# Performance work log

Hardware: AMD Instinct MI355X
Metric: run time of the kernel (lower is better)

Reference implementation:

```python
import jax, jax.numpy as jnp
import numpy as np

B, N, D, H, E, C = 32, 1024, 256, 256, 256, 256
K = 128          # top-k retained clusters = C // top_ratio
TEMP = 0.1
EPS = 1e-15


def _l2norm(x, eps=1e-12):
    n = jnp.linalg.norm(x, axis=-1, keepdims=True)
    return x / jnp.maximum(n, eps)


def _dense_sage(x, adj, Wr, br, Wo):
    # PyG DenseSAGEConv: mean-aggregate neighbors, lin_rel + lin_root, l2-normalize
    deg = jnp.clip(jnp.sum(adj, axis=-1, keepdims=True), 1.0, None)
    agg = jnp.matmul(adj, x) / deg                      # [B,N,D]
    out = agg @ Wr + br + x @ Wo                         # [B,N,H]
    return _l2norm(out)


def _sage_block(x, adj, Wr, br, Wo, Wl, bl):
    h = jax.nn.relu(_dense_sage(x, adj, Wr, br, Wo))
    return h @ Wl + bl


def setup_inputs() -> dict:
    key = jax.random.key(0)
    ks = jax.random.split(key, 12)
    sc = 0.05
    return {
        "x": jax.random.normal(ks[0], (B, N, D), jnp.float32),
        "adj": jax.random.uniform(ks[1], (B, N, N), jnp.float32),
        # pool branch (out = C clusters)
        "Wr_p": jax.random.normal(ks[2], (D, H), jnp.float32) * sc,
        "br_p": jnp.zeros((H,), jnp.float32),
        "Wo_p": jax.random.normal(ks[3], (D, H), jnp.float32) * sc,
        "Wl_p": jax.random.normal(ks[4], (H, C), jnp.float32) * sc,
        "bl_p": jnp.zeros((C,), jnp.float32),
        # embed branch (out = E features)
        "Wr_e": jax.random.normal(ks[5], (D, H), jnp.float32) * sc,
        "br_e": jnp.zeros((H,), jnp.float32),
        "Wo_e": jax.random.normal(ks[6], (D, H), jnp.float32) * sc,
        "Wl_e": jax.random.normal(ks[7], (H, E), jnp.float32) * sc,
        "bl_e": jnp.zeros((E,), jnp.float32),
    }


def reference(x, adj, Wr_p, br_p, Wo_p, Wl_p, bl_p, Wr_e, br_e, Wo_e, Wl_e, bl_e):
    s_logits = _sage_block(x, adj, Wr_p, br_p, Wo_p, Wl_p, bl_p)   # [B,N,C]
    node_x = _sage_block(x, adj, Wr_e, br_e, Wo_e, Wl_e, bl_e)     # [B,N,E]

    s = jax.nn.softmax(s_logits, axis=-1)

    # soft top-k cluster retain: sigmoid gate around the k-th largest column mass
    scores = jnp.sum(s, axis=1)                                    # [B,C]
    thresh = jax.lax.top_k(scores, K)[0][:, -1]                    # [B]
    gate = jax.nn.sigmoid((scores - thresh[:, None]) / TEMP)       # [B,C]
    s = s * gate[:, None, :]

    # pooled features / adjacency
    xp = jnp.einsum('bnc,bnd->bcd', s, node_x)                     # [B,C,E]
    sTa = jnp.einsum('bnc,bnm->bcm', s, adj)                       # [B,C,N]
    adj_p = jnp.einsum('bcm,bmk->bck', sTa, s)                     # [B,C,C]

    # link prediction loss: ||A - S S^T||_F / numel(A)
    ssT = jnp.einsum('bnc,bmc->bnm', s, s)
    link = jnp.linalg.norm(adj - ssT) / adj.size

    # entropy loss over assignments
    ent = jnp.mean(jnp.sum(-s * jnp.log(s + EPS), axis=-1))

    # cluster (orthogonality) loss: ||S^T S / ||S^T S||_F - I/sqrt(C)||_F
    sts = jnp.einsum('bnc,bnk->bck', s, s)                         # [B,C,C]
    sts_n = sts / jnp.maximum(
        jnp.linalg.norm(sts, axis=(-2, -1), keepdims=True), 1e-12)
    eye = jnp.eye(C, dtype=s.dtype) / jnp.sqrt(jnp.asarray(C, s.dtype))
    clu = jnp.mean(jnp.linalg.norm(sts_n - eye, axis=(-2, -1)))

    # adjacency reconstruction loss: ||A - S A_pool S^T||_F / numel(A)
    recon_adj = jnp.einsum('bnc,bck,bmk->bnm', s, adj_p, s)
    recon = jnp.linalg.norm(adj - recon_adj) / adj.size

    return (xp, adj_p, s, link, ent, clu, recon, node_x)
```

## Files before the change

### kernel.cpp

```cpp
#include <hip/hip_runtime.h>
#include <hip/hip_bf16.h>
#include <math.h>


typedef short bf16x8 __attribute__((ext_vector_type(8)));
typedef float f32x4 __attribute__((ext_vector_type(4)));

__device__ inline void gl_lds16(const void* g, void* l) {
    __builtin_amdgcn_global_load_lds(
        (const __attribute__((address_space(1))) void*)g,
        (__attribute__((address_space(3))) void*)l, 16, 0, 0);
}

__device__ inline unsigned short f2b(float f) {
    union { __hip_bfloat16 h; unsigned short u; } cv;
    cv.h = __float2bfloat16(f);
    return cv.u;
}
__device__ inline float b2f(unsigned short u) {
    union { unsigned short u; __hip_bfloat16 h; } cv;
    cv.u = u;
    return __bfloat162float(cv.h);
}

__global__ __launch_bounds__(256) void adjconv_kernel(
    const float* __restrict__ adj, unsigned short* __restrict__ adj_bf,
    float* __restrict__ deginv, float* __restrict__ asq_part) {
    __shared__ float sq_red[4];
    const int tid = threadIdx.x;
    const int wave = tid >> 6, lane = tid & 63;
    const long long row = (long long)blockIdx.x * 4 + wave;
    const float* ip = adj + row * 1024;
    unsigned short* op = adj_bf + row * 1024;
    float sum = 0.f, sq = 0.f;
#pragma unroll
    for (int i = 0; i < 4; ++i) {
        const float4 v = *(const float4*)(ip + i * 256 + lane * 4);
        ushort4 h;
        h.x = f2b(v.x); h.y = f2b(v.y); h.z = f2b(v.z); h.w = f2b(v.w);
        *(ushort4*)(op + i * 256 + lane * 4) = h;
        sum += v.x + v.y + v.z + v.w;
        sq = fmaf(v.x, v.x, sq);
        sq = fmaf(v.y, v.y, sq);
        sq = fmaf(v.z, v.z, sq);
        sq = fmaf(v.w, v.w, sq);
    }
#pragma unroll
    for (int off = 32; off > 0; off >>= 1) {
        sum += __shfl_xor(sum, off);
        sq  += __shfl_xor(sq, off);
    }
    if (lane == 0) {
        deginv[row] = 1.0f / fmaxf(sum, 1.0f);
        sq_red[wave] = sq;
    }
    __syncthreads();
    if (tid == 0)
        asq_part[blockIdx.x] = sq_red[0] + sq_red[1] + sq_red[2] + sq_red[3];
}

__global__ __launch_bounds__(256) void convt_kernel(
    const float* __restrict__ in, long long sIn, int ldin,
    unsigned short* __restrict__ outN, long long sN,
    unsigned short* __restrict__ outT, long long sT, int ldT,
    float* __restrict__ sqpart) {
    __shared__ float tile[64][65];
    __shared__ float sred[256];
    const int tid = threadIdx.x;
    const long long bz = blockIdx.z;
    const int rowBase = blockIdx.y * 64, colBase = blockIdx.x * 64;
    const float* ip = in + bz * sIn;
    float sq = 0.f;
#pragma unroll
    for (int i = 0; i < 4; ++i) {
        int r = (tid >> 4) * 4 + i;
        const float4 v = *(const float4*)(ip + (long long)(rowBase + r) * ldin + colBase + (tid & 15) * 4);
        tile[r][(tid & 15) * 4 + 0] = v.x;
        tile[r][(tid & 15) * 4 + 1] = v.y;
        tile[r][(tid & 15) * 4 + 2] = v.z;
        tile[r][(tid & 15) * 4 + 3] = v.w;
        if (outN) {
            ushort4 h;
            h.x = f2b(v.x); h.y = f2b(v.y); h.z = f2b(v.z); h.w = f2b(v.w);
            *(ushort4*)(outN + bz * sN + (long long)(rowBase + r) * ldin + colBase + (tid & 15) * 4) = h;
        }
        if (sqpart) sq += v.x * v.x + v.y * v.y + v.z * v.z + v.w * v.w;
    }
    __syncthreads();
    if (outT) {
#pragma unroll
        for (int i = 0; i < 4; ++i) {
            int oc = (tid >> 4) * 4 + i;
            ushort4 h;
            h.x = f2b(tile[(tid & 15) * 4 + 0][oc]);
            h.y = f2b(tile[(tid & 15) * 4 + 1][oc]);
            h.z = f2b(tile[(tid & 15) * 4 + 2][oc]);
            h.w = f2b(tile[(tid & 15) * 4 + 3][oc]);
            *(ushort4*)(outT + bz * sT + (long long)(colBase + oc) * ldT + rowBase + (tid & 15) * 4) = h;
        }
    }
    if (sqpart) {
        sred[tid] = sq;
        __syncthreads();
        for (int k = 128; k > 0; k >>= 1) {
            if (tid < k) sred[tid] += sred[tid + k];
            __syncthreads();
        }
        if (tid == 0)
            sqpart[((long long)bz * gridDim.y + blockIdx.y) * gridDim.x + blockIdx.x] = sred[0];
    }
}

__global__ __launch_bounds__(256) void tbf16_kernel(
    const unsigned short* __restrict__ in, long long sIn, int ldin,
    unsigned short* __restrict__ outT, long long sT, int ldT) {
    __shared__ unsigned short tile[64][68];
    const int tid = threadIdx.x;
    const long long bz = blockIdx.z;
    const int rowBase = blockIdx.y * 64, colBase = blockIdx.x * 64;
    const unsigned short* ip = in + bz * sIn;
#pragma unroll
    for (int i = 0; i < 4; ++i) {
        int r = (tid >> 4) * 4 + i, c4 = (tid & 15) * 4;
        ushort4 v = *(const ushort4*)(ip + (long long)(rowBase + r) * ldin + colBase + c4);
        tile[r][c4 + 0] = v.x; tile[r][c4 + 1] = v.y;
        tile[r][c4 + 2] = v.z; tile[r][c4 + 3] = v.w;
    }
    __syncthreads();
#pragma unroll
    for (int i = 0; i < 4; ++i) {
        int oc = (tid >> 4) * 4 + i;
        ushort4 h;
        h.x = tile[(tid & 15) * 4 + 0][oc];
        h.y = tile[(tid & 15) * 4 + 1][oc];
        h.z = tile[(tid & 15) * 4 + 2][oc];
        h.w = tile[(tid & 15) * 4 + 3][oc];
        *(ushort4*)(outT + bz * sT + (long long)(colBase + oc) * ldT + rowBase + (tid & 15) * 4) = h;
    }
}

struct WPtrs { const float* in[6]; unsigned short* out[6]; };
__global__ __launch_bounds__(256) void wconv_kernel(WPtrs wp) {
    __shared__ float tile[64][65];
    const int tid = threadIdx.x;
    const float* in = wp.in[blockIdx.z];
    unsigned short* out = wp.out[blockIdx.z];
    const int rowBase = blockIdx.y * 64, colBase = blockIdx.x * 64;
#pragma unroll
    for (int i = 0; i < 4; ++i) {
        int r = (tid >> 4) * 4 + i;
        const float4 v = *(const float4*)(in + (long long)(rowBase + r) * 256 + colBase + (tid & 15) * 4);
        tile[r][(tid & 15) * 4 + 0] = v.x;
        tile[r][(tid & 15) * 4 + 1] = v.y;
        tile[r][(tid & 15) * 4 + 2] = v.z;
        tile[r][(tid & 15) * 4 + 3] = v.w;
    }
    __syncthreads();
#pragma unroll
    for (int i = 0; i < 4; ++i) {
        int oc = (tid >> 4) * 4 + i;
        ushort4 h;
        h.x = f2b(tile[(tid & 15) * 4 + 0][oc]);
        h.y = f2b(tile[(tid & 15) * 4 + 1][oc]);
        h.z = f2b(tile[(tid & 15) * 4 + 2][oc]);
        h.w = f2b(tile[(tid & 15) * 4 + 3][oc]);
        *(ushort4*)(out + (long long)(colBase + oc) * 256 + rowBase + (tid & 15) * 4) = h;
    }
}

struct GemmP {
    const unsigned short* A1; long long sA1; int lda1; int K1;
    const unsigned short* B1; long long sB1; int ldb1;
    const unsigned short* A2; long long sA2; int lda2; int K2;
    const unsigned short* B2; long long sB2; int ldb2;
    float* outF; long long sF;
    unsigned short* outH; long long sH;
    int ldc;
    const float* bias;
    const float* rowscale; long long sRS;
    const float* dotT; long long sDot;
    float* dot_part;
};

__global__ __launch_bounds__(256) void gemm_mfma(GemmP p) {
    __shared__ short As[2][128 * 32];
    __shared__ short Bs[2][128 * 32];
    __shared__ float dred[256];
    const int tid = threadIdx.x;
    const int wave = tid >> 6, lane = tid & 63;
    const int quad = lane >> 4, l15 = lane & 15;
    const int wm = (wave & 1) * 64, wn = (wave >> 1) * 64;
    const long long bz = blockIdx.z;
    const int rowBase = blockIdx.y * 128, colBase = blockIdx.x * 128;
    const int srow = tid >> 2;
    const int skg = (((tid & 3) ^ ((srow >> 1) & 3)) * 8);
    const int rsw = (l15 >> 1) & 3;

    const int n1 = p.K1 >> 5;
    const int n2 = p.A2 ? (p.K2 >> 5) : 0;
    const int nTot = n1 + n2;

    const unsigned short* A1p = p.A1 + bz * p.sA1;
    const unsigned short* B1p = p.B1 + bz * p.sB1;
    const unsigned short* A2p = p.A2 ? p.A2 + bz * p.sA2 : nullptr;
    const unsigned short* B2p = p.B2 ? p.B2 + bz * p.sB2 : nullptr;

    auto stage = [&](int t, int buf) {
        const unsigned short *Ao, *Bo; int lda, ldb, ko;
        if (t < n1) { Ao = A1p; Bo = B1p; lda = p.lda1; ldb = p.ldb1; ko = t * 32; }
        else        { Ao = A2p; Bo = B2p; lda = p.lda2; ldb = p.ldb2; ko = (t - n1) * 32; }
        char* la = (char*)As + buf * 8192 + wave * 1024;
        char* lb = (char*)Bs + buf * 8192 + wave * 1024;
        gl_lds16(Ao + (long long)(rowBase + srow) * lda + ko + skg, la);
        gl_lds16(Ao + (long long)(rowBase + 64 + srow) * lda + ko + skg, la + 4096);
        gl_lds16(Bo + (long long)(colBase + srow) * ldb + ko + skg, lb);
        gl_lds16(Bo + (long long)(colBase + 64 + srow) * ldb + ko + skg, lb + 4096);
    };

    f32x4 acc[4][4] = {{{0.f}}};
    stage(0, 0);
    __syncthreads();
    int cur = 0;
    for (int t = 0; t < nTot; ++t) {
        if (t + 1 < nTot) stage(t + 1, cur ^ 1);
        const short* Ab = As[cur];
        const short* Bb = Bs[cur];
        bf16x8 af[4], bf[4];
#pragma unroll
        for (int i = 0; i < 4; ++i)
            af[i] = *(const bf16x8*)(Ab + (wm + i * 16 + l15) * 32 + (quad ^ rsw) * 8);
#pragma unroll
        for (int j = 0; j < 4; ++j)
            bf[j] = *(const bf16x8*)(Bb + (wn + j * 16 + l15) * 32 + (quad ^ rsw) * 8);
#pragma unroll
        for (int i = 0; i < 4; ++i)
#pragma unroll
            for (int j = 0; j < 4; ++j)
                acc[i][j] = __builtin_amdgcn_mfma_f32_16x16x32_bf16(af[i], bf[j], acc[i][j], 0, 0, 0);
        __syncthreads();
        cur ^= 1;
    }

    float* oF = p.outF ? p.outF + bz * p.sF : nullptr;
    unsigned short* oH = p.outH ? p.outH + bz * p.sH : nullptr;
    const float* dT = p.dotT ? p.dotT + bz * p.sDot : nullptr;
    float bcol[4];
#pragma unroll
    for (int j = 0; j < 4; ++j)
        bcol[j] = p.bias ? p.bias[colBase + wn + j * 16 + l15] : 0.0f;
    const float* rs = p.rowscale ? p.rowscale + bz * p.sRS : nullptr;
    float dacc = 0.f;
#pragma unroll
    for (int i = 0; i < 4; ++i) {
#pragma unroll
        for (int r = 0; r < 4; ++r) {
            int row = rowBase + wm + i * 16 + quad * 4 + r;
            float sc = rs ? rs[row] : 1.0f;
            long long ro = (long long)row * p.ldc;
#pragma unroll
            for (int j = 0; j < 4; ++j) {
                int col = colBase + wn + j * 16 + l15;
                float v = (acc[i][j][r] + bcol[j]) * sc;
                if (oF) oF[ro + col] = v;
                if (oH) oH[ro + col] = f2b(v);
                if (dT) dacc = fmaf(v, dT[(long long)col * p.ldc + row], dacc);
            }
        }
    }
    if (p.dot_part) {
        dred[tid] = dacc;
        __syncthreads();
        for (int k = 128; k > 0; k >>= 1) {
            if (tid < k) dred[tid] += dred[tid + k];
            __syncthreads();
        }
        if (tid == 0)
            p.dot_part[((long long)bz * gridDim.y + blockIdx.y) * gridDim.x + blockIdx.x] = dred[0];
    }
}

__global__ __launch_bounds__(256) void sts_clu_mfma(
    const unsigned short* __restrict__ sT, unsigned short* __restrict__ gout,
    float* __restrict__ ssq_part, float* __restrict__ tr_part) {
    __shared__ short As[2][128 * 32];
    __shared__ short Bs[2][128 * 32];
    __shared__ float red[2][256];
    const int tid = threadIdx.x;
    const int wave = tid >> 6, lane = tid & 63;
    const int quad = lane >> 4, l15 = lane & 15;
    const int wm = (wave & 1) * 64, wn = (wave >> 1) * 64;
    const long long bz = blockIdx.z;
    const unsigned short* S = sT + bz * 262144;
    const int rowBase = blockIdx.y * 128, colBase = blockIdx.x * 128;
    const int srow = tid >> 2;
    const int skg = (((tid & 3) ^ ((srow >> 1) & 3)) * 8);
    const int rsw = (l15 >> 1) & 3;

    auto stage = [&](int t, int buf) {
        int ko = t * 32;
        char* la = (char*)As + buf * 8192 + wave * 1024;
        char* lb = (char*)Bs + buf * 8192 + wave * 1024;
        gl_lds16(S + (long long)(rowBase + srow) * 1024 + ko + skg, la);
        gl_lds16(S + (long long)(rowBase + 64 + srow) * 1024 + ko + skg, la + 4096);
        gl_lds16(S + (long long)(colBase + srow) * 1024 + ko + skg, lb);
        gl_lds16(S + (long long)(colBase + 64 + srow) * 1024 + ko + skg, lb + 4096);
    };

    f32x4 acc[4][4] = {{{0.f}}};
    stage(0, 0);
    __syncthreads();
    int cur = 0;
    for (int t = 0; t < 32; ++t) {
        if (t + 1 < 32) stage(t + 1, cur ^ 1);
        const short* Ab = As[cur];
        const short* Bb = Bs[cur];
        bf16x8 af[4], bf[4];
#pragma unroll
        for (int i = 0; i < 4; ++i)
            af[i] = *(const bf16x8*)(Ab + (wm + i * 16 + l15) * 32 + (quad ^ rsw) * 8);
#pragma unroll
        for (int j = 0; j < 4; ++j)
            bf[j] = *(const bf16x8*)(Bb + (wn + j * 16 + l15) * 32 + (quad ^ rsw) * 8);
#pragma unroll
        for (int i = 0; i < 4; ++i)
#pragma unroll
            for (int j = 0; j < 4; ++j)
                acc[i][j] = __builtin_amdgcn_mfma_f32_16x16x32_bf16(af[i], bf[j], acc[i][j], 0, 0, 0);
        __syncthreads();
        cur ^= 1;
    }
    unsigned short* go = gout + bz * 65536;
    float ssq = 0.f, tr = 0.f;
#pragma unroll
    for (int i = 0; i < 4; ++i)
#pragma unroll
        for (int r = 0; r < 4; ++r) {
            int row = rowBase + wm + i * 16 + quad * 4 + r;
#pragma unroll
            for (int j = 0; j < 4; ++j) {
                int col = colBase + wn + j * 16 + l15;
                float v = acc[i][j][r];
                go[(long long)row * 256 + col] = f2b(v);
                ssq = fmaf(v, v, ssq);
                if (row == col) tr += v;
            }
        }
    red[0][tid] = ssq;
    red[1][tid] = tr;
    __syncthreads();
    for (int k = 128; k > 0; k >>= 1) {
        if (tid < k) {
            red[0][tid] += red[0][tid + k];
            red[1][tid] += red[1][tid + k];
        }
        __syncthreads();
    }
    if (tid == 0) {
        int bid = (int)(blockIdx.z * 4 + blockIdx.y * 2 + blockIdx.x);
        ssq_part[bid] = red[0][0];
        tr_part[bid] = red[1][0];
    }
}

__global__ __launch_bounds__(256) void dot_bf_kernel(const unsigned short* __restrict__ a,
                                                     const unsigned short* __restrict__ b,
                                                     float* __restrict__ part) {
    __shared__ float red[256];
    int tid = threadIdx.x;
    long long base = (long long)blockIdx.x * 8192;
    float acc = 0.f;
#pragma unroll
    for (int i = 0; i < 8; ++i) {
        long long off = base + i * 1024 + tid * 4;
        ushort4 va = *(const ushort4*)(a + off);
        ushort4 vb = *(const ushort4*)(b + off);
        acc = fmaf(b2f(va.x), b2f(vb.x), acc);
        acc = fmaf(b2f(va.y), b2f(vb.y), acc);
        acc = fmaf(b2f(va.z), b2f(vb.z), acc);
        acc = fmaf(b2f(va.w), b2f(vb.w), acc);
    }
    red[tid] = acc;
    __syncthreads();
    for (int k = 128; k > 0; k >>= 1) {
        if (tid < k) red[tid] += red[tid + k];
        __syncthreads();
    }
    if (tid == 0) part[blockIdx.x] = red[0];
}

__global__ __launch_bounds__(256) void l2relu_bf_kernel(unsigned short* __restrict__ buf) {
    __shared__ float red[256];
    long long row = blockIdx.x;
    int tid = threadIdx.x;
    float v = b2f(buf[row * 256 + tid]);
    red[tid] = v * v;
    __syncthreads();
    for (int k = 128; k > 0; k >>= 1) {
        if (tid < k) red[tid] += red[tid + k];
        __syncthreads();
    }
    float rn = 1.0f / fmaxf(sqrtf(red[0]), 1e-12f);
    buf[row * 256 + tid] = f2b(fmaxf(v * rn, 0.0f));
}

__global__ __launch_bounds__(256) void smstat_kernel(
    const float* __restrict__ s, float* __restrict__ rowmax,
    float* __restrict__ rowrden, float* __restrict__ scores) {
    __shared__ float sacc[4][256];
    const int tid = threadIdx.x;
    const int wave = tid >> 6, lane = tid & 63;
    const int b = blockIdx.x >> 5;
    const long long row0 = (long long)blockIdx.x * 32;
    float c0 = 0.f, c1 = 0.f, c2 = 0.f, c3 = 0.f;
#pragma unroll
    for (int q = 0; q < 8; ++q) {
        long long row = row0 + wave * 8 + q;
        const float4 v = *(const float4*)(s + row * 256 + lane * 4);
        float m = fmaxf(fmaxf(v.x, v.y), fmaxf(v.z, v.w));
#pragma unroll
        for (int off = 32; off > 0; off >>= 1) m = fmaxf(m, __shfl_xor(m, off));
        float e0 = expf(v.x - m), e1 = expf(v.y - m);
        float e2 = expf(v.z - m), e3 = expf(v.w - m);
        float den = e0 + e1 + e2 + e3;
#pragma unroll
        for (int off = 32; off > 0; off >>= 1) den += __shfl_xor(den, off);
        float rd = 1.0f / den;
        if (lane == 0) { rowmax[row] = m; rowrden[row] = rd; }
        c0 = fmaf(e0, rd, c0); c1 = fmaf(e1, rd, c1);
        c2 = fmaf(e2, rd, c2); c3 = fmaf(e3, rd, c3);
    }
    sacc[wave][lane * 4 + 0] = c0;
    sacc[wave][lane * 4 + 1] = c1;
    sacc[wave][lane * 4 + 2] = c2;
    sacc[wave][lane * 4 + 3] = c3;
    __syncthreads();
    float t0 = sacc[0][tid] + sacc[1][tid] + sacc[2][tid] + sacc[3][tid];
    atomicAdd(&scores[b * 256 + tid], t0);
}

__global__ __launch_bounds__(256) void topk_kernel(const float* __restrict__ scores,
                                                   float* __restrict__ thresh) {
    __shared__ float vals[256];
    int b = blockIdx.x, tid = threadIdx.x;
    float v = scores[b * 256 + tid];
    vals[tid] = v;
    __syncthreads();
    int rank = 0;
    for (int j = 0; j < 256; ++j) {
        float u = vals[j];
        rank += (u > v) || (u == v && j < tid);
    }
    if (rank == 127) thresh[b] = v;
}

__global__ __launch_bounds__(256) void gate_kernel(const float* __restrict__ scores,
                                                   const float* __restrict__ thresh,
                                                   float* __restrict__ gate) {
    int b = blockIdx.x, c = threadIdx.x;
    float z = (scores[b * 256 + c] - thresh[b]) * 10.0f;
    gate[b * 256 + c] = 1.0f / (1.0f + expf(-z));
}

__global__ __launch_bounds__(256) void gatefin_kernel(
    float* __restrict__ s, const float* __restrict__ rowmax,
    const float* __restrict__ rowrden, const float* __restrict__ gate,
    unsigned short* __restrict__ sbf, unsigned short* __restrict__ sT,
    float* __restrict__ ent_part) {
    __shared__ float tile[64][65];
    __shared__ float red[256];
    const int tid = threadIdx.x;
    const long long bz = blockIdx.z;
    const int rowBase = blockIdx.y * 64, colBase = blockIdx.x * 64;
    const int c4 = (tid & 15) * 4;
    const float g0 = gate[bz * 256 + colBase + c4 + 0];
    const float g1 = gate[bz * 256 + colBase + c4 + 1];
    const float g2 = gate[bz * 256 + colBase + c4 + 2];
    const float g3 = gate[bz * 256 + colBase + c4 + 3];
    float ent = 0.f;
#pragma unroll
    for (int i = 0; i < 4; ++i) {
        int r = (tid >> 4) * 4 + i;
        long long grow = bz * 1024 + rowBase + r;
        float4 v = *(const float4*)(s + grow * 256 + colBase + c4);
        float m = rowmax[grow], rd = rowrden[grow];
        float p0 = expf(v.x - m) * rd * g0;
        float p1 = expf(v.y - m) * rd * g1;
        float p2 = expf(v.z - m) * rd * g2;
        float p3 = expf(v.w - m) * rd * g3;
        float4 pv; pv.x = p0; pv.y = p1; pv.z = p2; pv.w = p3;
        *(float4*)(s + grow * 256 + colBase + c4) = pv;
        ushort4 h;
        h.x = f2b(p0); h.y = f2b(p1); h.z = f2b(p2); h.w = f2b(p3);
        *(ushort4*)(sbf + grow * 256 + colBase + c4) = h;
        tile[r][c4 + 0] = p0; tile[r][c4 + 1] = p1;
        tile[r][c4 + 2] = p2; tile[r][c4 + 3] = p3;
        ent -= p0 * logf(p0 + 1e-15f) + p1 * logf(p1 + 1e-15f) +
               p2 * logf(p2 + 1e-15f) + p3 * logf(p3 + 1e-15f);
    }
    __syncthreads();
#pragma unroll
    for (int i = 0; i < 4; ++i) {
        int oc = (tid >> 4) * 4 + i;
        ushort4 h;
        h.x = f2b(tile[c4 + 0][oc]);
        h.y = f2b(tile[c4 + 1][oc]);
        h.z = f2b(tile[c4 + 2][oc]);
        h.w = f2b(tile[c4 + 3][oc]);
        *(ushort4*)(sT + bz * 262144 + (long long)(colBase + oc) * 1024 + rowBase + c4) = h;
    }
    red[tid] = ent;
    __syncthreads();
    for (int k = 128; k > 0; k >>= 1) {
        if (tid < k) red[tid] += red[tid + k];
        __syncthreads();
    }
    if (tid == 0)
        ent_part[((long long)bz * gridDim.y + blockIdx.y) * gridDim.x + blockIdx.x] = red[0];
}

__global__ __launch_bounds__(256) void finalize_kernel(const float* __restrict__ ent_part,
                                                       const float* __restrict__ asq_part,
                                                       const float* __restrict__ psq_part,
                                                       const float* __restrict__ sdot_part,
                                                       const float* __restrict__ trq_part,
                                                       const float* __restrict__ ssq_part,
                                                       const float* __restrict__ tr_part,
                                                       float* __restrict__ scal) {
    __shared__ float red[7][256];
    int tid = threadIdx.x;
    float e = 0.f, asq = 0.f, psq = 0.f, sd = 0.f, tq = 0.f, clu = 0.f, ssqa = 0.f;
    for (int i = tid; i < 2048; i += 256) e += ent_part[i];
    for (int i = tid; i < 8192; i += 256) asq += asq_part[i];
    for (int i = tid; i < 512; i += 256) psq += psq_part[i];
    for (int i = tid; i < 1024; i += 256) sd += sdot_part[i];
    if (tid < 128) tq = trq_part[tid];
    if (tid < 32) {
        float ssq = 0.f, tr = 0.f;
#pragma unroll
        for (int i = 0; i < 4; ++i) {
            ssq += ssq_part[tid * 4 + i];
            tr  += tr_part[tid * 4 + i];
        }
        ssqa = ssq;
        float fro = fmaxf(sqrtf(ssq), 1e-12f);
        float val = ssq / (fro * fro) - tr / (8.0f * fro) + 1.0f;
        clu = sqrtf(fmaxf(val, 0.0f));
    }
    red[0][tid] = e; red[1][tid] = asq; red[2][tid] = psq; red[3][tid] = sd;
    red[4][tid] = tq; red[5][tid] = clu; red[6][tid] = ssqa;
    __syncthreads();
    for (int k = 128; k > 0; k >>= 1) {
        if (tid < k) {
#pragma unroll
            for (int q = 0; q < 7; ++q) red[q][tid] += red[q][tid + k];
        }
        __syncthreads();
    }
    if (tid == 0) {
        const float numel = 33554432.0f;
        float linksq  = red[1][0] - 2.0f * red[3][0] + red[6][0];
        float reconsq = red[1][0] - 2.0f * red[2][0] + red[4][0];
        scal[0] = sqrtf(fmaxf(linksq, 0.0f)) / numel;
        scal[1] = red[0][0] / 32768.0f;
        scal[2] = red[5][0] / 32.0f;
        scal[3] = sqrtf(fmaxf(reconsq, 0.0f)) / numel;
    }
}

extern "C" void kernel_launch(void* const* d_in, const int* in_sizes, int n_in,
                              void* d_out, int out_size, void* d_ws, size_t ws_size,
                              hipStream_t stream) {
    const float* x    = (const float*)d_in[0];
    const float* adj  = (const float*)d_in[1];
    const float* Wr_p = (const float*)d_in[2];
    const float* br_p = (const float*)d_in[3];
    const float* Wo_p = (const float*)d_in[4];
    const float* Wl_p = (const float*)d_in[5];
    const float* bl_p = (const float*)d_in[6];
    const float* Wr_e = (const float*)d_in[7];
    const float* br_e = (const float*)d_in[8];
    const float* Wo_e = (const float*)d_in[9];
    const float* Wl_e = (const float*)d_in[10];
    const float* bl_e = (const float*)d_in[11];

    float* out    = (float*)d_out;
    float* xp     = out;
    float* adj_p  = out + 2097152;
    float* s      = out + 4194304;
    float* scal   = out + 12582912;
    float* node_x = out + 12582916;

    char* w = (char*)d_ws;
    float* degsum     = (float*)w; w += 32768 * 4;
    float* scores     = (float*)w; w += 8192 * 4;
    float* thresh     = (float*)w; w += 256 * 4;
    float* gatep      = (float*)w; w += 8192 * 4;
    float* ent_part   = (float*)w; w += 32768 * 4;
    float* asq_part   = (float*)w; w += 8192 * 4;
    float* psq_part   = (float*)w; w += 512 * 4;
    float* sdot_part  = (float*)w; w += 1024 * 4;
    float* trq_part   = (float*)w; w += 256 * 4;
    float* ssq_part   = (float*)w; w += 256 * 4;
    float* tr_part    = (float*)w; w += 256 * 4;
    unsigned short* WT   = (unsigned short*)w; w += 6LL * 65536 * 2;
    unsigned short* bufA = (unsigned short*)w; w += 33554432LL * 2;
    unsigned short* bufB = (unsigned short*)w; w += 8388608LL * 2;
    unsigned short* bufC = (unsigned short*)w; w += 8388608LL * 2;
    unsigned short* bufD = (unsigned short*)w; w += 8388608LL * 2;
    unsigned short* bufE = (unsigned short*)w; w += 8388608LL * 2;
    unsigned short* bufF = (unsigned short*)w; w += 8388608LL * 2;
    unsigned short* bufG = (unsigned short*)w; w += 8388608LL * 2;
    unsigned short* bufH = (unsigned short*)w; w += 2097152LL * 2;

    unsigned short* G_bf  = bufB;
    unsigned short* PT_bf = bufB + 2097152;
    float*          M1    = (float*)(bufB + 4194304);
    float* rowmax  = degsum;
    float* rowrden = (float*)bufH;

    hipMemsetAsync(scores, 0, 8192 * sizeof(float), stream);

    adjconv_kernel<<<8192, 256, 0, stream>>>(adj, bufA, degsum, asq_part);

    convt_kernel<<<dim3(4, 16, 32), 256, 0, stream>>>(
        x, 262144LL, 256, bufB, 262144LL, bufC, 262144LL, 1024, nullptr);

    WPtrs wp;
    wp.in[0] = Wr_p; wp.in[1] = Wo_p; wp.in[2] = Wl_p;
    wp.in[3] = Wr_e; wp.in[4] = Wo_e; wp.in[5] = Wl_e;
    for (int i = 0; i < 6; ++i) wp.out[i] = WT + (long long)i * 65536;
    wconv_kernel<<<dim3(4, 4, 6), 256, 0, stream>>>(wp);

    GemmP g;
    g = {};
    g.A1 = bufA; g.sA1 = 1048576; g.lda1 = 1024; g.K1 = 1024;
    g.B1 = bufC; g.sB1 = 262144; g.ldb1 = 1024;
    g.outH = bufD; g.sH = 262144; g.ldc = 256;
    g.rowscale = degsum; g.sRS = 1024;
    gemm_mfma<<<dim3(2, 8, 32), 256, 0, stream>>>(g);

    g = {};
    g.A1 = bufD; g.sA1 = 0; g.lda1 = 256; g.K1 = 256; g.B1 = WT + 0 * 65536; g.sB1 = 0; g.ldb1 = 256;
    g.A2 = bufB; g.sA2 = 0; g.lda2 = 256; g.K2 = 256; g.B2 = WT + 1 * 65536; g.sB2 = 0; g.ldb2 = 256;
    g.outH = bufE; g.sH = 0; g.ldc = 256; g.bias = br_p;
    gemm_mfma<<<dim3(2, 256, 1), 256, 0, stream>>>(g);
    l2relu_bf_kernel<<<32768, 256, 0, stream>>>(bufE);

    g = {};
    g.A1 = bufE; g.sA1 = 0; g.lda1 = 256; g.K1 = 256; g.B1 = WT + 2 * 65536; g.sB1 = 0; g.ldb1 = 256;
    g.outF = s; g.sF = 0; g.ldc = 256; g.bias = bl_p;
    gemm_mfma<<<dim3(2, 256, 1), 256, 0, stream>>>(g);

    g = {};
    g.A1 = bufD; g.sA1 = 0; g.lda1 = 256; g.K1 = 256; g.B1 = WT + 3 * 65536; g.sB1 = 0; g.ldb1 = 256;
    g.A2 = bufB; g.sA2 = 0; g.lda2 = 256; g.K2 = 256; g.B2 = WT + 4 * 65536; g.sB2 = 0; g.ldb2 = 256;
    g.outH = bufE; g.sH = 0; g.ldc = 256; g.bias = br_e;
    gemm_mfma<<<dim3(2, 256, 1), 256, 0, stream>>>(g);
    l2relu_bf_kernel<<<32768, 256, 0, stream>>>(bufE);
    g = {};
    g.A1 = bufE; g.sA1 = 0; g.lda1 = 256; g.K1 = 256; g.B1 = WT + 5 * 65536; g.sB1 = 0; g.ldb1 = 256;
    g.outF = node_x; g.sF = 0; g.outH = bufF; g.sH = 0; g.ldc = 256; g.bias = bl_e;
    gemm_mfma<<<dim3(2, 256, 1), 256, 0, stream>>>(g);

    smstat_kernel<<<1024, 256, 0, stream>>>(s, rowmax, rowrden, scores);
    topk_kernel<<<32, 256, 0, stream>>>(scores, thresh);
    gate_kernel<<<32, 256, 0, stream>>>(scores, thresh, gatep);
    gatefin_kernel<<<dim3(4, 16, 32), 256, 0, stream>>>(
        s, rowmax, rowrden, gatep, bufG, bufC, ent_part);

    tbf16_kernel<<<dim3(4, 16, 32), 256, 0, stream>>>(
        bufF, 262144LL, 256, bufD, 262144LL, 1024);

    g = {};
    g.A1 = bufC; g.sA1 = 262144; g.lda1 = 1024; g.K1 = 1024;
    g.B1 = bufD; g.sB1 = 262144; g.ldb1 = 1024;
    g.outF = xp; g.sF = 65536; g.ldc = 256;
    gemm_mfma<<<dim3(2, 2, 32), 256, 0, stream>>>(g);

    g = {};
    g.A1 = bufA; g.sA1 = 1048576; g.lda1 = 1024; g.K1 = 1024;
    g.B1 = bufC; g.sB1 = 262144; g.ldb1 = 1024;
    g.outH = bufE; g.sH = 262144; g.ldc = 256;
    gemm_mfma<<<dim3(2, 8, 32), 256, 0, stream>>>(g);

    tbf16_kernel<<<dim3(4, 16, 32), 256, 0, stream>>>(
        bufE, 262144LL, 256, bufF, 262144LL, 1024);

    sts_clu_mfma<<<dim3(2, 2, 32), 256, 0, stream>>>(bufC, G_bf, ssq_part, tr_part);

    g = {};
    g.A1 = bufC; g.sA1 = 262144; g.lda1 = 1024; g.K1 = 1024;
    g.B1 = bufF; g.sB1 = 262144; g.ldb1 = 1024;
    g.outF = adj_p; g.sF = 65536; g.ldc = 256;
    gemm_mfma<<<dim3(2, 2, 32), 256, 0, stream>>>(g);

    convt_kernel<<<dim3(4, 4, 32), 256, 0, stream>>>(
        adj_p, 65536LL, 256, bufH, 65536LL, PT_bf, 65536LL, 256, psq_part);

    dot_bf_kernel<<<1024, 256, 0, stream>>>(bufG, bufE, sdot_part);

    g = {};
    g.A1 = G_bf; g.sA1 = 65536; g.lda1 = 256; g.K1 = 256;
    g.B1 = PT_bf; g.sB1 = 65536; g.ldb1 = 256;
    g.outF = M1; g.sF = 65536; g.ldc = 256;
    gemm_mfma<<<dim3(2, 2, 32), 256, 0, stream>>>(g);

    g = {};
    g.A1 = G_bf; g.sA1 = 65536; g.lda1 = 256; g.K1 = 256;
    g.B1 = bufH; g.sB1 = 65536; g.ldb1 = 256;
    g.ldc = 256;
    g.dotT = M1; g.sDot = 65536; g.dot_part = trq_part;
    gemm_mfma<<<dim3(2, 2, 32), 256, 0, stream>>>(g);

    finalize_kernel<<<1, 256, 0, stream>>>(ent_part, asq_part, psq_part, sdot_part,
                                           trq_part, ssq_part, tr_part, scal);
}
```

Measured before the change: 665.7 us.

## Fuse L2-norm/ReLU into SAGE GEMM and transposes, dot, and reductions into GEMM epilogues

```diff
diff --git a/kernel.cpp b/kernel.cpp
--- a/kernel.cpp
+++ b/kernel.cpp
@@ -5,6 +5,7 @@
 
 typedef short bf16x8 __attribute__((ext_vector_type(8)));
 typedef float f32x4 __attribute__((ext_vector_type(4)));
+typedef unsigned short u16x8 __attribute__((ext_vector_type(8)));
 
 __device__ inline void gl_lds16(const void* g, void* l) {
     __builtin_amdgcn_global_load_lds(
@@ -34,16 +35,18 @@
     unsigned short* op = adj_bf + row * 1024;
     float sum = 0.f, sq = 0.f;
 #pragma unroll
-    for (int i = 0; i < 4; ++i) {
-        const float4 v = *(const float4*)(ip + i * 256 + lane * 4);
-        ushort4 h;
-        h.x = f2b(v.x); h.y = f2b(v.y); h.z = f2b(v.z); h.w = f2b(v.w);
-        *(ushort4*)(op + i * 256 + lane * 4) = h;
-        sum += v.x + v.y + v.z + v.w;
-        sq = fmaf(v.x, v.x, sq);
-        sq = fmaf(v.y, v.y, sq);
-        sq = fmaf(v.z, v.z, sq);
-        sq = fmaf(v.w, v.w, sq);
+    for (int i = 0; i < 2; ++i) {
+        const float4 v0 = *(const float4*)(ip + i * 512 + lane * 8);
+        const float4 v1 = *(const float4*)(ip + i * 512 + lane * 8 + 4);
+        u16x8 h;
+        h[0] = f2b(v0.x); h[1] = f2b(v0.y); h[2] = f2b(v0.z); h[3] = f2b(v0.w);
+        h[4] = f2b(v1.x); h[5] = f2b(v1.y); h[6] = f2b(v1.z); h[7] = f2b(v1.w);
+        *(u16x8*)(op + i * 512 + lane * 8) = h;
+        sum += (v0.x + v0.y + v0.z + v0.w) + (v1.x + v1.y + v1.z + v1.w);
+        sq = fmaf(v0.x, v0.x, sq); sq = fmaf(v0.y, v0.y, sq);
+        sq = fmaf(v0.z, v0.z, sq); sq = fmaf(v0.w, v0.w, sq);
+        sq = fmaf(v1.x, v1.x, sq); sq = fmaf(v1.y, v1.y, sq);
+        sq = fmaf(v1.z, v1.z, sq); sq = fmaf(v1.w, v1.w, sq);
     }
 #pragma unroll
     for (int off = 32; off > 0; off >>= 1) {
@@ -62,15 +65,12 @@
 __global__ __launch_bounds__(256) void convt_kernel(
     const float* __restrict__ in, long long sIn, int ldin,
     unsigned short* __restrict__ outN, long long sN,
-    unsigned short* __restrict__ outT, long long sT, int ldT,
-    float* __restrict__ sqpart) {
+    unsigned short* __restrict__ outT, long long sT, int ldT) {
     __shared__ float tile[64][65];
-    __shared__ float sred[256];
     const int tid = threadIdx.x;
     const long long bz = blockIdx.z;
     const int rowBase = blockIdx.y * 64, colBase = blockIdx.x * 64;
     const float* ip = in + bz * sIn;
-    float sq = 0.f;
 #pragma unroll
     for (int i = 0; i < 4; ++i) {
         int r = (tid >> 4) * 4 + i;
@@ -84,7 +84,6 @@
             h.x = f2b(v.x); h.y = f2b(v.y); h.z = f2b(v.z); h.w = f2b(v.w);
             *(ushort4*)(outN + bz * sN + (long long)(rowBase + r) * ldin + colBase + (tid & 15) * 4) = h;
         }
-        if (sqpart) sq += v.x * v.x + v.y * v.y + v.z * v.z + v.w * v.w;
     }
     __syncthreads();
     if (outT) {
@@ -99,44 +98,6 @@
             *(ushort4*)(outT + bz * sT + (long long)(colBase + oc) * ldT + rowBase + (tid & 15) * 4) = h;
         }
     }
-    if (sqpart) {
-        sred[tid] = sq;
-        __syncthreads();
-        for (int k = 128; k > 0; k >>= 1) {
-            if (tid < k) sred[tid] += sred[tid + k];
-            __syncthreads();
-        }
-        if (tid == 0)
-            sqpart[((long long)bz * gridDim.y + blockIdx.y) * gridDim.x + blockIdx.x] = sred[0];
-    }
-}
-
-__global__ __launch_bounds__(256) void tbf16_kernel(
-    const unsigned short* __restrict__ in, long long sIn, int ldin,
-    unsigned short* __restrict__ outT, long long sT, int ldT) {
-    __shared__ unsigned short tile[64][68];
-    const int tid = threadIdx.x;
-    const long long bz = blockIdx.z;
-    const int rowBase = blockIdx.y * 64, colBase = blockIdx.x * 64;
-    const unsigned short* ip = in + bz * sIn;
-#pragma unroll
-    for (int i = 0; i < 4; ++i) {
-        int r = (tid >> 4) * 4 + i, c4 = (tid & 15) * 4;
-        ushort4 v = *(const ushort4*)(ip + (long long)(rowBase + r) * ldin + colBase + c4);
-        tile[r][c4 + 0] = v.x; tile[r][c4 + 1] = v.y;
-        tile[r][c4 + 2] = v.z; tile[r][c4 + 3] = v.w;
-    }
-    __syncthreads();
-#pragma unroll
-    for (int i = 0; i < 4; ++i) {
-        int oc = (tid >> 4) * 4 + i;
-        ushort4 h;
-        h.x = tile[(tid & 15) * 4 + 0][oc];
-        h.y = tile[(tid & 15) * 4 + 1][oc];
-        h.z = tile[(tid & 15) * 4 + 2][oc];
-        h.w = tile[(tid & 15) * 4 + 3][oc];
-        *(ushort4*)(outT + bz * sT + (long long)(colBase + oc) * ldT + rowBase + (tid & 15) * 4) = h;
-    }
 }
 
 struct WPtrs { const float* in[6]; unsigned short* out[6]; };
@@ -175,16 +136,17 @@
     const unsigned short* B2; long long sB2; int ldb2;
     float* outF; long long sF;
     unsigned short* outH; long long sH;
+    unsigned short* outT; long long sT; int ldt;
     int ldc;
     const float* bias;
     const float* rowscale; long long sRS;
-    const float* dotT; long long sDot;
+    const unsigned short* dotN; long long sDot;
     float* dot_part;
+    float* sq_part;
 };
 
 __global__ __launch_bounds__(256) void gemm_mfma(GemmP p) {
-    __shared__ short As[2][128 * 32];
-    __shared__ short Bs[2][128 * 32];
+    __shared__ char smem[32768];
     __shared__ float dred[256];
     const int tid = threadIdx.x;
     const int wave = tid >> 6, lane = tid & 63;
@@ -209,8 +171,8 @@
         const unsigned short *Ao, *Bo; int lda, ldb, ko;
         if (t < n1) { Ao = A1p; Bo = B1p; lda = p.lda1; ldb = p.ldb1; ko = t * 32; }
         else        { Ao = A2p; Bo = B2p; lda = p.lda2; ldb = p.ldb2; ko = (t - n1) * 32; }
-        char* la = (char*)As + buf * 8192 + wave * 1024;
-        char* lb = (char*)Bs + buf * 8192 + wave * 1024;
+        char* la = smem + buf * 16384 + wave * 1024;
+        char* lb = smem + buf * 16384 + 8192 + wave * 1024;
         gl_lds16(Ao + (long long)(rowBase + srow) * lda + ko + skg, la);
         gl_lds16(Ao + (long long)(rowBase + 64 + srow) * lda + ko + skg, la + 4096);
         gl_lds16(Bo + (long long)(colBase + srow) * ldb + ko + skg, lb);
@@ -223,8 +185,8 @@
     int cur = 0;
     for (int t = 0; t < nTot; ++t) {
         if (t + 1 < nTot) stage(t + 1, cur ^ 1);
-        const short* Ab = As[cur];
-        const short* Bb = Bs[cur];
+        const short* Ab = (const short*)(smem + cur * 16384);
+        const short* Bb = (const short*)(smem + cur * 16384 + 8192);
         bf16x8 af[4], bf[4];
 #pragma unroll
         for (int i = 0; i < 4; ++i)
@@ -243,7 +205,8 @@
 
     float* oF = p.outF ? p.outF + bz * p.sF : nullptr;
     unsigned short* oH = p.outH ? p.outH + bz * p.sH : nullptr;
-    const float* dT = p.dotT ? p.dotT + bz * p.sDot : nullptr;
+    const unsigned short* dN = p.dotN ? p.dotN + bz * p.sDot : nullptr;
+    unsigned short* tt = (unsigned short*)smem;
     float bcol[4];
 #pragma unroll
     for (int j = 0; j < 4; ++j)
@@ -252,6 +215,7 @@
     float dacc = 0.f;
 #pragma unroll
     for (int i = 0; i < 4; ++i) {
+        ushort4 tp[4];
 #pragma unroll
         for (int r = 0; r < 4; ++r) {
             int row = rowBase + wm + i * 16 + quad * 4 + r;
@@ -263,20 +227,136 @@
                 float v = (acc[i][j][r] + bcol[j]) * sc;
                 if (oF) oF[ro + col] = v;
                 if (oH) oH[ro + col] = f2b(v);
-                if (dT) dacc = fmaf(v, dT[(long long)col * p.ldc + row], dacc);
+                if (dN) dacc = fmaf(v, b2f(dN[ro + col]), dacc);
+                if (p.sq_part) dacc = fmaf(v, v, dacc);
+                ((unsigned short*)&tp[j])[r] = f2b(v);
             }
         }
-    }
-    if (p.dot_part) {
+        if (p.outT) {
+            int lr = wm + i * 16 + quad * 4;
+#pragma unroll
+            for (int j = 0; j < 4; ++j) {
+                int lc = wn + j * 16 + l15;
+                *(ushort4*)&tt[lc * 128 + (lr ^ ((lc & 15) << 3))] = tp[j];
+            }
+        }
+    }
+    if (p.outT) {
+        __syncthreads();
+#pragma unroll
+        for (int u = 0; u < 8; ++u) {
+            int idx = u * 256 + tid;
+            int c = idx >> 4;
+            int r0 = (idx & 15) * 8;
+            u16x8 val = *(const u16x8*)&tt[c * 128 + (r0 ^ ((c & 15) << 3))];
+            int gr = rowBase + r0;
+            long long tb = bz + (gr >> 10);
+            *(u16x8*)(p.outT + tb * p.sT + (long long)(colBase + c) * p.ldt + (gr & 1023)) = val;
+        }
+    }
+    if (p.dot_part || p.sq_part) {
         dred[tid] = dacc;
         __syncthreads();
         for (int k = 128; k > 0; k >>= 1) {
             if (tid < k) dred[tid] += dred[tid + k];
             __syncthreads();
         }
-        if (tid == 0)
-            p.dot_part[((long long)bz * gridDim.y + blockIdx.y) * gridDim.x + blockIdx.x] = dred[0];
-    }
+        if (tid == 0) {
+            float* dst = p.dot_part ? p.dot_part : p.sq_part;
+            dst[((long long)bz * gridDim.y + blockIdx.y) * gridDim.x + blockIdx.x] = dred[0];
+        }
+    }
+}
+
+struct SageP {
+    const unsigned short* A1; const unsigned short* B1;
+    const unsigned short* A2; const unsigned short* B2;
+    const float* bias;
+    unsigned short* out;
+};
+
+__global__ __launch_bounds__(512) void sage_mfma(SageP p) {
+    __shared__ short As[2][4096];
+    __shared__ short Bs[2][8192];
+    __shared__ float rsum[4][128];
+    const int tid = threadIdx.x;
+    const int wave = tid >> 6, lane = tid & 63;
+    const int quad = lane >> 4, l15 = lane & 15;
+    const int wm = (wave & 1) * 64, wn = (wave >> 1) * 64;
+    const int rowBase = blockIdx.x * 128;
+    const int srow = tid >> 2;
+    const int skg = (((tid & 3) ^ ((srow >> 1) & 3)) * 8);
+    const int rsw = (l15 >> 1) & 3;
+
+    auto stage = [&](int t, int buf) {
+        const unsigned short* Ao = (t < 8) ? p.A1 : p.A2;
+        const unsigned short* Bo = (t < 8) ? p.B1 : p.B2;
+        int ko = (t & 7) * 32;
+        char* la = (char*)As[buf] + wave * 1024;
+        char* lb = (char*)Bs[buf] + wave * 1024;
+        gl_lds16(Ao + (long long)(rowBase + srow) * 256 + ko + skg, la);
+        gl_lds16(Bo + (long long)srow * 256 + ko + skg, lb);
+        gl_lds16(Bo + (long long)(128 + srow) * 256 + ko + skg, lb + 8192);
+    };
+
+    f32x4 acc[4][4] = {{{0.f}}};
+    stage(0, 0);
+    __syncthreads();
+    int cur = 0;
+    for (int t = 0; t < 16; ++t) {
+        if (t + 1 < 16) stage(t + 1, cur ^ 1);
+        const short* Ab = As[cur];
+        const short* Bb = Bs[cur];
+        bf16x8 af[4], bf[4];
+#pragma unroll
+        for (int i = 0; i < 4; ++i)
+            af[i] = *(const bf16x8*)(Ab + (wm + i * 16 + l15) * 32 + (quad ^ rsw) * 8);
+#pragma unroll
+        for (int j = 0; j < 4; ++j)
+            bf[j] = *(const bf16x8*)(Bb + (wn + j * 16 + l15) * 32 + (quad ^ rsw) * 8);
+#pragma unroll
+        for (int i = 0; i < 4; ++i)
+#pragma unroll
+            for (int j = 0; j < 4; ++j)
+                acc[i][j] = __builtin_amdgcn_mfma_f32_16x16x32_bf16(af[i], bf[j], acc[i][j], 0, 0, 0);
+        __syncthreads();
+        cur ^= 1;
+    }
+
+    float bcol[4];
+#pragma unroll
+    for (int j = 0; j < 4; ++j)
+        bcol[j] = p.bias[wn + j * 16 + l15];
+
+#pragma unroll
+    for (int i = 0; i < 4; ++i)
+#pragma unroll
+        for (int r = 0; r < 4; ++r) {
+            float ss = 0.f;
+#pragma unroll
+            for (int j = 0; j < 4; ++j) {
+                float v = acc[i][j][r] + bcol[j];
+                ss = fmaf(v, v, ss);
+            }
+#pragma unroll
+            for (int off = 1; off < 16; off <<= 1) ss += __shfl_xor(ss, off);
+            if (l15 == 0) rsum[wave >> 1][wm + i * 16 + quad * 4 + r] = ss;
+        }
+    __syncthreads();
+#pragma unroll
+    for (int i = 0; i < 4; ++i)
+#pragma unroll
+        for (int r = 0; r < 4; ++r) {
+            int lrow = wm + i * 16 + quad * 4 + r;
+            float tot = rsum[0][lrow] + rsum[1][lrow] + rsum[2][lrow] + rsum[3][lrow];
+            float rn = 1.0f / fmaxf(sqrtf(tot), 1e-12f);
+            long long ro = (long long)(rowBase + lrow) * 256;
+#pragma unroll
+            for (int j = 0; j < 4; ++j) {
+                float v = (acc[i][j][r] + bcol[j]) * rn;
+                p.out[ro + wn + j * 16 + l15] = f2b(fmaxf(v, 0.0f));
+            }
+        }
 }
 
 __global__ __launch_bounds__(256) void sts_clu_mfma(
@@ -312,8 +392,8 @@
     int cur = 0;
     for (int t = 0; t < 32; ++t) {
         if (t + 1 < 32) stage(t + 1, cur ^ 1);
-        const short* Ab = As[cur];
-        const short* Bb = Bs[cur];
+        const short* Ab = (const short*)((char*)As + cur * 8192);
+        const short* Bb = (const short*)((char*)Bs + cur * 8192);
         bf16x8 af[4], bf[4];
 #pragma unroll
         for (int i = 0; i < 4; ++i)
@@ -362,45 +442,82 @@
     }
 }
 
-__global__ __launch_bounds__(256) void dot_bf_kernel(const unsigned short* __restrict__ a,
-                                                     const unsigned short* __restrict__ b,
-                                                     float* __restrict__ part) {
-    __shared__ float red[256];
-    int tid = threadIdx.x;
-    long long base = (long long)blockIdx.x * 8192;
-    float acc = 0.f;
-#pragma unroll
-    for (int i = 0; i < 8; ++i) {
-        long long off = base + i * 1024 + tid * 4;
-        ushort4 va = *(const ushort4*)(a + off);
-        ushort4 vb = *(const ushort4*)(b + off);
-        acc = fmaf(b2f(va.x), b2f(vb.x), acc);
-        acc = fmaf(b2f(va.y), b2f(vb.y), acc);
-        acc = fmaf(b2f(va.z), b2f(vb.z), acc);
-        acc = fmaf(b2f(va.w), b2f(vb.w), acc);
-    }
-    red[tid] = acc;
+__global__ __launch_bounds__(256) void trq_mfma(
+    const unsigned short* __restrict__ G, const unsigned short* __restrict__ P,
+    const unsigned short* __restrict__ PT, float* __restrict__ trq_part) {
+    __shared__ short sm[4][2][4096];
+    __shared__ float dred[256];
+    const int tid = threadIdx.x;
+    const int wave = tid >> 6, lane = tid & 63;
+    const int quad = lane >> 4, l15 = lane & 15;
+    const int wm = (wave & 1) * 64, wn = (wave >> 1) * 64;
+    const long long bz = blockIdx.z;
+    const int rowBase = blockIdx.y * 128, colBase = blockIdx.x * 128;
+    const int srow = tid >> 2;
+    const int skg = (((tid & 3) ^ ((srow >> 1) & 3)) * 8);
+    const int rsw = (l15 >> 1) & 3;
+    const unsigned short* Gb = G + bz * 65536;
+    const unsigned short* Pb = P + bz * 65536;
+    const unsigned short* PTb = PT + bz * 65536;
+
+    auto stage = [&](int t, int buf) {
+        int ko = t * 32;
+#pragma unroll
+        for (int h = 0; h < 2; ++h) {
+            int rr = rowBase + h * 64 + srow, cc = colBase + h * 64 + srow;
+            gl_lds16(Gb + (long long)rr * 256 + ko + skg, (char*)sm[0][buf] + h * 4096 + wave * 1024);
+            gl_lds16(PTb + (long long)cc * 256 + ko + skg, (char*)sm[1][buf] + h * 4096 + wave * 1024);
+            gl_lds16(Pb + (long long)rr * 256 + ko + skg, (char*)sm[2][buf] + h * 4096 + wave * 1024);
+            gl_lds16(Gb + (long long)cc * 256 + ko + skg, (char*)sm[3][buf] + h * 4096 + wave * 1024);
+        }
+    };
+
+    f32x4 a1[4][4] = {{{0.f}}};
+    f32x4 a3[4][4] = {{{0.f}}};
+    stage(0, 0);
+    __syncthreads();
+    int cur = 0;
+    for (int t = 0; t < 8; ++t) {
+        if (t + 1 < 8) stage(t + 1, cur ^ 1);
+        bf16x8 gA[4], pB[4], pA[4], gB[4];
+#pragma unroll
+        for (int i = 0; i < 4; ++i) {
+            int ro = (wm + i * 16 + l15) * 32 + (quad ^ rsw) * 8;
+            gA[i] = *(const bf16x8*)(sm[0][cur] + ro);
+            pA[i] = *(const bf16x8*)(sm[2][cur] + ro);
+        }
+#pragma unroll
+        for (int j = 0; j < 4; ++j) {
+            int co = (wn + j * 16 + l15) * 32 + (quad ^ rsw) * 8;
+            pB[j] = *(const bf16x8*)(sm[1][cur] + co);
+            gB[j] = *(const bf16x8*)(sm[3][cur] + co);
+        }
+#pragma unroll
+        for (int i = 0; i < 4; ++i)
+#pragma unroll
+            for (int j = 0; j < 4; ++j) {
+                a1[i][j] = __builtin_amdgcn_mfma_f32_16x16x32_bf16(gA[i], pB[j], a1[i][j], 0, 0, 0);
+                a3[i][j] = __builtin_amdgcn_mfma_f32_16x16x32_bf16(pA[i], gB[j], a3[i][j], 0, 0, 0);
+            }
+        __syncthreads();
+        cur ^= 1;
+    }
+    float dacc = 0.f;
+#pragma unroll
+    for (int i = 0; i < 4; ++i)
+#pragma unroll
+        for (int j = 0; j < 4; ++j)
+#pragma unroll
+            for (int r = 0; r < 4; ++r)
+                dacc = fmaf(a3[i][j][r], a1[i][j][r], dacc);
+    dred[tid] = dacc;
     __syncthreads();
     for (int k = 128; k > 0; k >>= 1) {
-        if (tid < k) red[tid] += red[tid + k];
-        __syncthreads();
-    }
-    if (tid == 0) part[blockIdx.x] = red[0];
-}
-
-__global__ __launch_bounds__(256) void l2relu_bf_kernel(unsigned short* __restrict__ buf) {
-    __shared__ float red[256];
-    long long row = blockIdx.x;
-    int tid = threadIdx.x;
-    float v = b2f(buf[row * 256 + tid]);
-    red[tid] = v * v;
-    __syncthreads();
-    for (int k = 128; k > 0; k >>= 1) {
-        if (tid < k) red[tid] += red[tid + k];
-        __syncthreads();
-    }
-    float rn = 1.0f / fmaxf(sqrtf(red[0]), 1e-12f);
-    buf[row * 256 + tid] = f2b(fmaxf(v * rn, 0.0f));
+        if (tid < k) dred[tid] += dred[tid + k];
+        __syncthreads();
+    }
+    if (tid == 0)
+        trq_part[(blockIdx.z * 2 + blockIdx.y) * 2 + blockIdx.x] = dred[0];
 }
 
 __global__ __launch_bounds__(256) void smstat_kernel(
@@ -438,9 +555,10 @@
     atomicAdd(&scores[b * 256 + tid], t0);
 }
 
-__global__ __launch_bounds__(256) void topk_kernel(const float* __restrict__ scores,
-                                                   float* __restrict__ thresh) {
+__global__ __launch_bounds__(256) void topkgate_kernel(const float* __restrict__ scores,
+                                                       float* __restrict__ gate) {
     __shared__ float vals[256];
+    __shared__ float th;
     int b = blockIdx.x, tid = threadIdx.x;
     float v = scores[b * 256 + tid];
     vals[tid] = v;
@@ -450,15 +568,10 @@
         float u = vals[j];
         rank += (u > v) || (u == v && j < tid);
     }
-    if (rank == 127) thresh[b] = v;
-}
-
-__global__ __launch_bounds__(256) void gate_kernel(const float* __restrict__ scores,
-                                                   const float* __restrict__ thresh,
-                                                   float* __restrict__ gate) {
-    int b = blockIdx.x, c = threadIdx.x;
-    float z = (scores[b * 256 + c] - thresh[b]) * 10.0f;
-    gate[b * 256 + c] = 1.0f / (1.0f + expf(-z));
+    if (rank == 127) th = v;
+    __syncthreads();
+    float z = (v - th) * 10.0f;
+    gate[b * 256 + tid] = 1.0f / (1.0f + expf(-z));
 }
 
 __global__ __launch_bounds__(256) void gatefin_kernel(
@@ -531,8 +644,8 @@
     float e = 0.f, asq = 0.f, psq = 0.f, sd = 0.f, tq = 0.f, clu = 0.f, ssqa = 0.f;
     for (int i = tid; i < 2048; i += 256) e += ent_part[i];
     for (int i = tid; i < 8192; i += 256) asq += asq_part[i];
-    for (int i = tid; i < 512; i += 256) psq += psq_part[i];
-    for (int i = tid; i < 1024; i += 256) sd += sdot_part[i];
+    if (tid < 128) psq = psq_part[tid];
+    for (int i = tid; i < 512; i += 256) sd += sdot_part[i];
     if (tid < 128) tq = trq_part[tid];
     if (tid < 32) {
         float ssq = 0.f, tr = 0.f;
@@ -614,16 +727,16 @@
 
     unsigned short* G_bf  = bufB;
     unsigned short* PT_bf = bufB + 2097152;
-    float*          M1    = (float*)(bufB + 4194304);
     float* rowmax  = degsum;
     float* rowrden = (float*)bufH;
+    (void)thresh;
 
     hipMemsetAsync(scores, 0, 8192 * sizeof(float), stream);
 
     adjconv_kernel<<<8192, 256, 0, stream>>>(adj, bufA, degsum, asq_part);
 
     convt_kernel<<<dim3(4, 16, 32), 256, 0, stream>>>(
-        x, 262144LL, 256, bufB, 262144LL, bufC, 262144LL, 1024, nullptr);
+        x, 262144LL, 256, bufB, 262144LL, bufC, 262144LL, 1024);
 
     WPtrs wp;
     wp.in[0] = Wr_p; wp.in[1] = Wo_p; wp.in[2] = Wl_p;
@@ -639,37 +752,32 @@
     g.rowscale = degsum; g.sRS = 1024;
     gemm_mfma<<<dim3(2, 8, 32), 256, 0, stream>>>(g);
 
-    g = {};
-    g.A1 = bufD; g.sA1 = 0; g.lda1 = 256; g.K1 = 256; g.B1 = WT + 0 * 65536; g.sB1 = 0; g.ldb1 = 256;
-    g.A2 = bufB; g.sA2 = 0; g.lda2 = 256; g.K2 = 256; g.B2 = WT + 1 * 65536; g.sB2 = 0; g.ldb2 = 256;
-    g.outH = bufE; g.sH = 0; g.ldc = 256; g.bias = br_p;
-    gemm_mfma<<<dim3(2, 256, 1), 256, 0, stream>>>(g);
-    l2relu_bf_kernel<<<32768, 256, 0, stream>>>(bufE);
+    SageP sp;
+    sp.A1 = bufD; sp.B1 = WT + 0 * 65536;
+    sp.A2 = bufB; sp.B2 = WT + 1 * 65536;
+    sp.bias = br_p; sp.out = bufE;
+    sage_mfma<<<256, 512, 0, stream>>>(sp);
 
     g = {};
     g.A1 = bufE; g.sA1 = 0; g.lda1 = 256; g.K1 = 256; g.B1 = WT + 2 * 65536; g.sB1 = 0; g.ldb1 = 256;
     g.outF = s; g.sF = 0; g.ldc = 256; g.bias = bl_p;
     gemm_mfma<<<dim3(2, 256, 1), 256, 0, stream>>>(g);
 
-    g = {};
-    g.A1 = bufD; g.sA1 = 0; g.lda1 = 256; g.K1 = 256; g.B1 = WT + 3 * 65536; g.sB1 = 0; g.ldb1 = 256;
-    g.A2 = bufB; g.sA2 = 0; g.lda2 = 256; g.K2 = 256; g.B2 = WT + 4 * 65536; g.sB2 = 0; g.ldb2 = 256;
-    g.outH = bufE; g.sH = 0; g.ldc = 256; g.bias = br_e;
-    gemm_mfma<<<dim3(2, 256, 1), 256, 0, stream>>>(g);
-    l2relu_bf_kernel<<<32768, 256, 0, stream>>>(bufE);
+    sp.A1 = bufD; sp.B1 = WT + 3 * 65536;
+    sp.A2 = bufB; sp.B2 = WT + 4 * 65536;
+    sp.bias = br_e; sp.out = bufE;
+    sage_mfma<<<256, 512, 0, stream>>>(sp);
+
     g = {};
     g.A1 = bufE; g.sA1 = 0; g.lda1 = 256; g.K1 = 256; g.B1 = WT + 5 * 65536; g.sB1 = 0; g.ldb1 = 256;
-    g.outF = node_x; g.sF = 0; g.outH = bufF; g.sH = 0; g.ldc = 256; g.bias = bl_e;
+    g.outF = node_x; g.sF = 0; g.ldc = 256; g.bias = bl_e;
+    g.outT = bufD; g.sT = 262144; g.ldt = 1024;
     gemm_mfma<<<dim3(2, 256, 1), 256, 0, stream>>>(g);
 
     smstat_kernel<<<1024, 256, 0, stream>>>(s, rowmax, rowrden, scores);
-    topk_kernel<<<32, 256, 0, stream>>>(scores, thresh);
-    gate_kernel<<<32, 256, 0, stream>>>(scores, thresh, gatep);
+    topkgate_kernel<<<32, 256, 0, stream>>>(scores, gatep);
     gatefin_kernel<<<dim3(4, 16, 32), 256, 0, stream>>>(
         s, rowmax, rowrden, gatep, bufG, bufC, ent_part);
-
-    tbf16_kernel<<<dim3(4, 16, 32), 256, 0, stream>>>(
-        bufF, 262144LL, 256, bufD, 262144LL, 1024);
 
     g = {};
     g.A1 = bufC; g.sA1 = 262144; g.lda1 = 1024; g.K1 = 1024;
@@ -680,11 +788,10 @@
     g = {};
     g.A1 = bufA; g.sA1 = 1048576; g.lda1 = 1024; g.K1 = 1024;
     g.B1 = bufC; g.sB1 = 262144; g.ldb1 = 1024;
-    g.outH = bufE; g.sH = 262144; g.ldc = 256;
+    g.ldc = 256;
+    g.outT = bufF; g.sT = 262144; g.ldt = 1024;
+    g.dotN = bufG; g.sDot = 262144; g.dot_part = sdot_part;
     gemm_mfma<<<dim3(2, 8, 32), 256, 0, stream>>>(g);
-
-    tbf16_kernel<<<dim3(4, 16, 32), 256, 0, stream>>>(
-        bufE, 262144LL, 256, bufF, 262144LL, 1024);
 
     sts_clu_mfma<<<dim3(2, 2, 32), 256, 0, stream>>>(bufC, G_bf, ssq_part, tr_part);
 
@@ -692,25 +799,12 @@
     g.A1 = bufC; g.sA1 = 262144; g.lda1 = 1024; g.K1 = 1024;
     g.B1 = bufF; g.sB1 = 262144; g.ldb1 = 1024;
     g.outF = adj_p; g.sF = 65536; g.ldc = 256;
+    g.outH = bufH; g.sH = 65536;
+    g.outT = PT_bf; g.sT = 65536; g.ldt = 256;
+    g.sq_part = psq_part;
     gemm_mfma<<<dim3(2, 2, 32), 256, 0, stream>>>(g);
 
-    convt_kernel<<<dim3(4, 4, 32), 256, 0, stream>>>(
-        adj_p, 65536LL, 256, bufH, 65536LL, PT_bf, 65536LL, 256, psq_part);
-
-    dot_bf_kernel<<<1024, 256, 0, stream>>>(bufG, bufE, sdot_part);
-
-    g = {};
-    g.A1 = G_bf; g.sA1 = 65536; g.lda1 = 256; g.K1 = 256;
-    g.B1 = PT_bf; g.sB1 = 65536; g.ldb1 = 256;
-    g.outF = M1; g.sF = 65536; g.ldc = 256;
-    gemm_mfma<<<dim3(2, 2, 32), 256, 0, stream>>>(g);
-
-    g = {};
-    g.A1 = G_bf; g.sA1 = 65536; g.lda1 = 256; g.K1 = 256;
-    g.B1 = bufH; g.sB1 = 65536; g.ldb1 = 256;
-    g.ldc = 256;
-    g.dotT = M1; g.sDot = 65536; g.dot_part = trq_part;
-    gemm_mfma<<<dim3(2, 2, 32), 256, 0, stream>>>(g);
+    trq_mfma<<<dim3(2, 2, 32), 256, 0, stream>>>(G_bf, bufH, PT_bf, trq_part);
 
     finalize_kernel<<<1, 256, 0, stream>>>(ent_part, asq_part, psq_part, sdot_part,
                                            trq_part, ssq_part, tr_part, scal);
```

After: 580.0 us. -12.9%, faster.
